# Performance work log

Hardware: AMD Instinct MI355X
Metric: run time of the kernel (lower is better)

Reference implementation:

```python
import jax, jax.numpy as jnp
import numpy as np

EPS = 0.1
MAX_ITER = 100
THRESH = 0.1


def setup_inputs() -> dict:
    key = jax.random.key(0)
    k1, k2, k3, k4 = jax.random.split(key, 4)
    N, P1, P2, D = 4, 1024, 1024, 16
    x = jax.random.normal(k1, (N, P1, D), dtype=jnp.float32)
    y = jax.random.normal(k2, (N, P2, D), dtype=jnp.float32)
    wx = jax.random.uniform(k3, (N, P1), dtype=jnp.float32)
    wy = jax.random.uniform(k4, (N, P2), dtype=jnp.float32)
    # normalize to probability weights (typical usage for empirical measures)
    wx = wx / jnp.sum(wx, axis=-1, keepdims=True)
    wy = wy / jnp.sum(wy, axis=-1, keepdims=True)
    return {"x": x, "y": y, "wx": wx, "wy": wy}


def _cost_matrix(x, y):
    # |x_i - y_j|^1 summed over feature dim -> [N, P1, P2]
    return jnp.sum(jnp.abs(x[:, :, None, :] - y[:, None, :, :]), axis=-1)


def reference(x, y, wx, wy):
    C = _cost_matrix(x, y)                     # [N, P1, P2]
    mu, nu = wx, wy                            # [N, P1], [N, P2]
    log_mu = jnp.log(mu + 1e-8)
    log_nu = jnp.log(nu + 1e-8)

    def M(u, v):
        # (-C_ij + u_i + v_j) / eps
        return (-C + u[:, :, None] + v[:, None, :]) / EPS

    def step(carry, _):
        u, v, done = carry
        u_new = EPS * (log_mu - jax.nn.logsumexp(M(u, v), axis=-1)) + u
        v_new = EPS * (log_nu - jax.nn.logsumexp(M(u_new, v), axis=-2)) + v
        err = jnp.mean(jnp.sum(jnp.abs(u_new - u), axis=-1))
        # emulate torch's early break: freeze u,v once converged
        u_out = jnp.where(done, u, u_new)
        v_out = jnp.where(done, v, v_new)
        done = done | (err < THRESH)
        return (u_out, v_out, done), None

    u0 = jnp.zeros_like(mu)
    v0 = jnp.zeros_like(nu)
    (u, v, _), _ = jax.lax.scan(step, (u0, v0, jnp.array(False)), None, length=MAX_ITER)

    pi = jnp.exp(M(u, v))                      # transport plan [N, P1, P2]
    cost = jnp.sum(pi * C, axis=(-2, -1))      # [N]  (reduction='none')
    return cost, pi, C
```

## Files before the change

kernel.cpp:

```cpp
#include <hip/hip_runtime.h>

static constexpr int   NB      = 4;
static constexpr int   PP      = 1024;
static constexpr int   DD      = 16;
static constexpr float EPSV    = 0.1f;
static constexpr float KE      = 14.42695041f;
static constexpr float KL      = 0.0693147181f;
static constexpr int   MAXIT   = 100;
static constexpr float THRESHV = 0.1f;

static constexpr int NBLK = 256;
static constexpr int NTHR = 512;
static constexpr unsigned DONEG = 1000000u;

static constexpr int    ERR_F_OFF     = 4352;
static constexpr size_t WS_ZERO_BYTES = 4352 * 4;
static constexpr size_t ERR_BYTES     = 512 * 4;

static constexpr int    VSNAP_OFF = 131072;
static constexpr int    CNT_F_OFF = 786432;
static constexpr size_t CNT_BYTES = (size_t)2 * MAXIT * 64;

__device__ __forceinline__ float fexp2(float v) { return __builtin_amdgcn_exp2f(v); }
__device__ __forceinline__ float flog2(float v) { return __builtin_amdgcn_logf(v); }

__device__ __forceinline__ float aload(const float* p) {
    return __hip_atomic_load(p, __ATOMIC_RELAXED, __HIP_MEMORY_SCOPE_AGENT);
}
__device__ __forceinline__ void astore(float* p, float v) {
    __hip_atomic_store(p, v, __ATOMIC_RELAXED, __HIP_MEMORY_SCOPE_AGENT);
}
__device__ __forceinline__ unsigned aloadu(const unsigned* p) {
    return __hip_atomic_load(p, __ATOMIC_RELAXED, __HIP_MEMORY_SCOPE_AGENT);
}
__device__ __forceinline__ void astoreu(unsigned* p, unsigned v) {
    __hip_atomic_store(p, v, __ATOMIC_RELAXED, __HIP_MEMORY_SCOPE_AGENT);
}
__device__ __forceinline__ float2 aload2(const float* p) {
    unsigned long long v = __hip_atomic_load((const unsigned long long*)p,
                                             __ATOMIC_RELAXED, __HIP_MEMORY_SCOPE_AGENT);
    union { unsigned long long u; float f[2]; } c; c.u = v;
    return make_float2(c.f[0], c.f[1]);
}
__device__ __forceinline__ void astore2(float* p, float a, float b) {
    union { unsigned long long u; float f[2]; } c; c.f[0] = a; c.f[1] = b;
    __hip_atomic_store((unsigned long long*)p, c.u,
                       __ATOMIC_RELAXED, __HIP_MEMORY_SCOPE_AGENT);
}
__device__ __forceinline__ void aadd(unsigned* p, unsigned v) {
    (void)__hip_atomic_fetch_add(p, v, __ATOMIC_RELAXED, __HIP_MEMORY_SCOPE_AGENT);
}

__device__ __forceinline__ void gbar_group(unsigned* ws32, int n, int g, unsigned gen) {
    __syncthreads();
    if (threadIdx.x < 64) {
        if (threadIdx.x == 0) astoreu(ws32 + (n * 64 + g) * 16, gen);
        const unsigned* sp = ws32 + (n * 64 + threadIdx.x) * 16;
        while (__ballot(aloadu(sp) >= gen) != ~0ull)
            __builtin_amdgcn_s_sleep(1);
    }
    __syncthreads();
}

__global__ __launch_bounds__(NTHR, 2)
void sinkhorn_kernel(const float* __restrict__ x, const float* __restrict__ y,
                     const float* __restrict__ wx, const float* __restrict__ wy,
                     float* __restrict__ out, float* __restrict__ ws)
{
    __shared__ float rt[16 * PP];
    __shared__ float sbuf[PP];
    __shared__ float cred[8];
    __shared__ int   Ts;
    __shared__ int   s_ex;
    __shared__ int   s_fired;

    unsigned* ws32  = (unsigned*)ws;
    unsigned* Tslot = ws32 + 4096;
    float*    ews   = ws + ERR_F_OFF;

    float* out_cost = out;
    float* out_pi   = out + NB;
    float* out_C    = out + NB + (size_t)NB * PP * PP;

    const int b   = blockIdx.x;
    const int n   = b >> 6;
    const int g   = b & 63;
    const int i0  = g * 16;
    const int w   = threadIdx.x >> 6;
    const int l   = threadIdx.x & 63;
    const int tid = threadIdx.x;

    float* sc = out_C + (size_t)n * PP * PP;
    unsigned* cnt = (unsigned*)(sc + CNT_F_OFF);

    if (tid == 0) { s_ex = 0; s_fired = 0; }

    float4 xr[2][4];
    #pragma unroll
    for (int rr = 0; rr < 2; ++rr) {
        const float4* xp = (const float4*)(x + ((size_t)n * PP + (i0 + 2 * w + rr)) * DD);
        #pragma unroll
        for (int q = 0; q < 4; ++q) xr[rr][q] = xp[q];
    }
    #pragma unroll 4
    for (int k = 0; k < 16; ++k) {
        int j = l + 64 * k;
        const float4* yp = (const float4*)(y + ((size_t)n * PP + j) * DD);
        float4 y0 = yp[0], y1 = yp[1], y2 = yp[2], y3 = yp[3];
        #pragma unroll
        for (int rr = 0; rr < 2; ++rr) {
            float c = fabsf(xr[rr][0].x - y0.x) + fabsf(xr[rr][0].y - y0.y)
                    + fabsf(xr[rr][0].z - y0.z) + fabsf(xr[rr][0].w - y0.w)
                    + fabsf(xr[rr][1].x - y1.x) + fabsf(xr[rr][1].y - y1.y)
                    + fabsf(xr[rr][1].z - y1.z) + fabsf(xr[rr][1].w - y1.w)
                    + fabsf(xr[rr][2].x - y2.x) + fabsf(xr[rr][2].y - y2.y)
                    + fabsf(xr[rr][2].z - y2.z) + fabsf(xr[rr][2].w - y2.w)
                    + fabsf(xr[rr][3].x - y3.x) + fabsf(xr[rr][3].y - y3.y)
                    + fabsf(xr[rr][3].z - y3.z) + fabsf(xr[rr][3].w - y3.w);
            rt[(2 * w + rr) * PP + j] = c;
        }
    }

    float4 yc[2][4];
    #pragma unroll
    for (int c = 0; c < 2; ++c) {
        const float4* yp = (const float4*)(y + ((size_t)n * PP + (i0 + 2 * w + c)) * DD);
        #pragma unroll
        for (int q = 0; q < 4; ++q) yc[c][q] = yp[q];
    }
    float2 c2[16];
    #pragma unroll 4
    for (int k = 0; k < 16; ++k) {
        const float4* xp = (const float4*)(x + ((size_t)n * PP + (l + 64 * k)) * DD);
        float4 x0 = xp[0], x1 = xp[1], x2 = xp[2], x3 = xp[3];
        float cc[2];
        #pragma unroll
        for (int c = 0; c < 2; ++c) {
            cc[c] = fabsf(x0.x - yc[c][0].x) + fabsf(x0.y - yc[c][0].y)
                  + fabsf(x0.z - yc[c][0].z) + fabsf(x0.w - yc[c][0].w)
                  + fabsf(x1.x - yc[c][1].x) + fabsf(x1.y - yc[c][1].y)
                  + fabsf(x1.z - yc[c][1].z) + fabsf(x1.w - yc[c][1].w)
                  + fabsf(x2.x - yc[c][2].x) + fabsf(x2.y - yc[c][2].y)
                  + fabsf(x2.z - yc[c][2].z) + fabsf(x2.w - yc[c][2].w)
                  + fabsf(x3.x - yc[c][3].x) + fabsf(x3.y - yc[c][3].y)
                  + fabsf(x3.z - yc[c][3].z) + fabsf(x3.w - yc[c][3].w);
        }
        c2[k] = make_float2(cc[0], cc[1]);
    }

    float lmu[2], lnu[2];
    #pragma unroll
    for (int rr = 0; rr < 2; ++rr) {
        lmu[rr] = __logf(wx[n * PP + i0 + 2 * w + rr] + 1e-8f);
        lnu[rr] = __logf(wy[n * PP + i0 + 2 * w + rr] + 1e-8f);
    }

    float uprev0 = 0.f, uprev1 = 0.f;

    #pragma unroll 1
    for (int t = 0; t < MAXIT; ++t) {
        if (t == 0) {
            sbuf[2 * tid] = 0.f; sbuf[2 * tid + 1] = 0.f;
        } else {
            if (tid == 0) {
                const unsigned* cp = cnt + (unsigned)(2 * (t - 1) + 1) * 16;
                unsigned cv;
                while (((cv = aloadu(cp)) & 0xFFFFu) != 64u)
                    __builtin_amdgcn_s_sleep(1);
                s_ex = (int)(cv >> 16);
            }
            __syncthreads();
            if (s_ex != 0) break;
            float2 vp = aload2(sc + VSNAP_OFF + (size_t)(t - 1) * PP + 2 * tid);
            sbuf[2 * tid] = vp.x; sbuf[2 * tid + 1] = vp.y;
        }
        __syncthreads();

        {
            float4 tt[2][4];
            float m0 = -3.4e38f, m1 = -3.4e38f;
            #pragma unroll
            for (int k = 0; k < 4; ++k) {
                int j = 256 * k + 4 * l;
                float4 v4 = *(const float4*)&sbuf[j];
                float4 ca = *(const float4*)&rt[(2 * w) * PP + j];
                float4 cb = *(const float4*)&rt[(2 * w + 1) * PP + j];
                tt[0][k] = make_float4(v4.x - ca.x, v4.y - ca.y, v4.z - ca.z, v4.w - ca.w);
                tt[1][k] = make_float4(v4.x - cb.x, v4.y - cb.y, v4.z - cb.z, v4.w - cb.w);
                m0 = fmaxf(m0, fmaxf(fmaxf(tt[0][k].x, tt[0][k].y), fmaxf(tt[0][k].z, tt[0][k].w)));
                m1 = fmaxf(m1, fmaxf(fmaxf(tt[1][k].x, tt[1][k].y), fmaxf(tt[1][k].z, tt[1][k].w)));
            }
            #pragma unroll
            for (int off = 32; off >= 1; off >>= 1) {
                m0 = fmaxf(m0, __shfl_xor(m0, off));
                m1 = fmaxf(m1, __shfl_xor(m1, off));
            }
            float s0 = 0.f, s1 = 0.f;
            #pragma unroll
            for (int k = 0; k < 4; ++k) {
                s0 += fexp2((tt[0][k].x - m0) * KE) + fexp2((tt[0][k].y - m0) * KE)
                    + fexp2((tt[0][k].z - m0) * KE) + fexp2((tt[0][k].w - m0) * KE);
                s1 += fexp2((tt[1][k].x - m1) * KE) + fexp2((tt[1][k].y - m1) * KE)
                    + fexp2((tt[1][k].z - m1) * KE) + fexp2((tt[1][k].w - m1) * KE);
            }
            #pragma unroll
            for (int off = 32; off >= 1; off >>= 1) {
                s0 += __shfl_xor(s0, off);
                s1 += __shfl_xor(s1, off);
            }
            float un0 = EPSV * lmu[0] - (m0 + KL * flog2(s0));
            float un1 = EPSV * lmu[1] - (m1 + KL * flog2(s1));
            if (l == 0) astore2(sc + (size_t)t * PP + i0 + 2 * w, un0, un1);
        }
        __syncthreads();
        if (tid == 0) {
            unsigned* cp = cnt + (unsigned)(2 * t) * 16;
            aadd(cp, 1u);
            while ((aloadu(cp) & 0xFFFFu) != 64u) __builtin_amdgcn_s_sleep(1);
        }
        __syncthreads();

        {
            float2 up = aload2(sc + (size_t)t * PP + 2 * tid);
            sbuf[2 * tid] = up.x; sbuf[2 * tid + 1] = up.y;
            float we = fabsf(up.x - uprev0) + fabsf(up.y - uprev1);
            uprev0 = up.x; uprev1 = up.y;
            #pragma unroll
            for (int off = 32; off >= 1; off >>= 1) we += __shfl_xor(we, off);
            if (l == 0) cred[w] = we;
        }
        __syncthreads();

        {
            float tt0[16], tt1[16], m0 = -3.4e38f, m1 = -3.4e38f;
            #pragma unroll
            for (int k = 0; k < 16; ++k) {
                float uu = sbuf[l + 64 * k];
                tt0[k] = uu - c2[k].x;
                tt1[k] = uu - c2[k].y;
                m0 = fmaxf(m0, tt0[k]);
                m1 = fmaxf(m1, tt1[k]);
            }
            #pragma unroll
            for (int off = 32; off >= 1; off >>= 1) {
                m0 = fmaxf(m0, __shfl_xor(m0, off));
                m1 = fmaxf(m1, __shfl_xor(m1, off));
            }
            float s0 = 0.f, s1 = 0.f;
            #pragma unroll
            for (int k = 0; k < 16; ++k) {
                s0 += fexp2((tt0[k] - m0) * KE);
                s1 += fexp2((tt1[k] - m1) * KE);
            }
            #pragma unroll
            for (int off = 32; off >= 1; off >>= 1) {
                s0 += __shfl_xor(s0, off);
                s1 += __shfl_xor(s1, off);
            }
            float vn0 = EPSV * lnu[0] - (m0 + KL * flog2(s0));
            float vn1 = EPSV * lnu[1] - (m1 + KL * flog2(s1));
            if (l == 0)
                astore2(sc + VSNAP_OFF + (size_t)t * PP + i0 + 2 * w, vn0, vn1);
        }
        if (g == 0 && tid == 0) {
            float es = cred[0] + cred[1] + cred[2] + cred[3]
                     + cred[4] + cred[5] + cred[6] + cred[7];
            astore(ews + n * 128 + t, es);
        }
        if (g == 0 && s_fired == 0 && tid < 64) {
            float esl = cred[0] + cred[1] + cred[2] + cred[3]
                      + cred[4] + cred[5] + cred[6] + cred[7];
            float s1f = 0.f, s2f = 0.f;
            #pragma unroll
            for (int q = 0; q < NB; ++q) {
                float e1 = aload(ews + q * 128 + tid);
                float e2 = aload(ews + q * 128 + 64 + tid);
                if (q == n) {
                    if (tid == t)      e1 = esl;
                    if (64 + tid == t) e2 = esl;
                }
                s1f += e1; s2f += e2;
            }
            unsigned long long bb = __ballot(s1f < THRESHV * (float)NB)
                                  | __ballot(s2f < THRESHV * (float)NB);
            if (tid == 0 && bb != 0ull) s_fired = 1;
        }

        __syncthreads();
        if (tid == 0) {
            unsigned addv = 1u + ((g == 0 && s_fired != 0) ? 65536u : 0u);
            aadd(cnt + (unsigned)(2 * t + 1) * 16, addv);
        }
    }

    if (g == 0 && tid == 0) astoreu(ws32 + (n * 64) * 16, DONEG);

    if (b == 0 && tid < 64) {
        for (;;) {
            bool ok = (tid >= 4) || (aloadu(ws32 + tid * 64 * 16) >= DONEG);
            if (__ballot(ok) == ~0ull) break;
            __builtin_amdgcn_s_sleep(2);
        }
        float s1f = aload(ews + 0 * 128 + tid) + aload(ews + 1 * 128 + tid)
                  + aload(ews + 2 * 128 + tid) + aload(ews + 3 * 128 + tid);
        float s2f = aload(ews + 0 * 128 + 64 + tid) + aload(ews + 1 * 128 + 64 + tid)
                  + aload(ews + 2 * 128 + 64 + tid) + aload(ews + 3 * 128 + 64 + tid);
        unsigned long long b1 = __ballot(s1f < THRESHV * (float)NB);
        unsigned long long b2 = __ballot(s2f < THRESHV * (float)NB);
        int T = b1 ? (__ffsll((long long)b1) - 1)
                   : (b2 ? 64 + (__ffsll((long long)b2) - 1) : MAXIT - 1);
        if (tid == 0) astoreu(Tslot, (unsigned)(T + 1));
    }
    if (tid == 0) {
        unsigned tv;
        while ((tv = aloadu(Tslot)) == 0u) __builtin_amdgcn_s_sleep(2);
        Ts = (int)tv - 1;
    }
    __syncthreads();
    const int T = Ts;

    float u_loc[2];
    {
        float2 up = aload2(sc + (size_t)T * PP + i0 + 2 * w);
        u_loc[0] = up.x; u_loc[1] = up.y;
        float2 vp = aload2(sc + VSNAP_OFF + (size_t)T * PP + 2 * tid);
        sbuf[2 * tid] = vp.x; sbuf[2 * tid + 1] = vp.y;
    }
    gbar_group(ws32, n, g, DONEG + 1u);

    float cacc = 0.f;
    #pragma unroll
    for (int rr = 0; rr < 2; ++rr) {
        int r = 2 * w + rr;
        int i = i0 + r;
        float un = u_loc[rr];
        #pragma unroll
        for (int k = 0; k < 4; ++k) {
            int j = 256 * k + 4 * l;
            float4 c4 = *(const float4*)&rt[r * PP + j];
            float4 v4 = *(const float4*)&sbuf[j];
            float4 p4;
            p4.x = fexp2((un + v4.x - c4.x) * KE);
            p4.y = fexp2((un + v4.y - c4.y) * KE);
            p4.z = fexp2((un + v4.z - c4.z) * KE);
            p4.w = fexp2((un + v4.w - c4.w) * KE);
            *(float4*)&out_pi[((size_t)n * PP + i) * PP + j] = p4;
            *(float4*)&out_C [((size_t)n * PP + i) * PP + j] = c4;
            cacc += p4.x * c4.x + p4.y * c4.y + p4.z * c4.z + p4.w * c4.w;
        }
    }
    #pragma unroll
    for (int off = 32; off >= 1; off >>= 1) cacc += __shfl_xor(cacc, off);
    if (l == 0) cred[w] = cacc;
    __syncthreads();
    if (tid == 0) {
        float s = 0.f;
        #pragma unroll
        for (int q = 0; q < 8; ++q) s += cred[q];
        atomicAdd(&out_cost[n], s);
    }
}

extern "C" void kernel_launch(void* const* d_in, const int* in_sizes, int n_in,
                              void* d_out, int out_size, void* d_ws, size_t ws_size,
                              hipStream_t stream) {
    const float* x  = (const float*)d_in[0];
    const float* y  = (const float*)d_in[1];
    const float* wx = (const float*)d_in[2];
    const float* wy = (const float*)d_in[3];
    float* out = (float*)d_out;
    float* ws  = (float*)d_ws;

    (void)hipMemsetAsync(d_ws, 0, WS_ZERO_BYTES, stream);
    (void)hipMemsetAsync((char*)d_ws + WS_ZERO_BYTES, 0x7f, ERR_BYTES, stream);
    (void)hipMemsetAsync(d_out, 0, NB * sizeof(float), stream);
    {
        size_t out_C_off = ((size_t)NB + (size_t)NB * PP * PP) * sizeof(float);
        size_t start = out_C_off + (size_t)CNT_F_OFF * sizeof(float);
        size_t span  = (size_t)(NB - 1) * PP * PP * sizeof(float) + CNT_BYTES;
        (void)hipMemsetAsync((char*)d_out + start, 0, span, stream);
    }

    hipLaunchKernelGGL(sinkhorn_kernel, dim3(NBLK), dim3(NTHR), 0, stream,
                       x, y, wx, wy, out, ws);
}
```

Before: 842.2 us.

## Replace counter barriers with NaN-sentinel dataflow sync and swizzled shared staging

Drops the per-iteration atomic counter barriers between the u and v half-steps. The snapshot buffers are now prefilled with 0xFF (NaN), and consumers poll until every value they need is non-NaN, so each block waits only on data arrival and not on a group-wide counter. Early exit now goes through a per-batch exit flag that blocks check with a one-iteration lag. Shared-memory staging of u and v uses XOR-swizzled indices to avoid bank conflicts. In exchange it adds a larger memset of the scratch area and spin polling on many addresses.

Result: slower. 998.0 us (+18.5%).

```diff
diff --git a/kernel.cpp b/kernel.cpp
--- a/kernel.cpp
+++ b/kernel.cpp
@@ -17,9 +17,8 @@
 static constexpr size_t WS_ZERO_BYTES = 4352 * 4;
 static constexpr size_t ERR_BYTES     = 512 * 4;
 
-static constexpr int    VSNAP_OFF = 131072;
-static constexpr int    CNT_F_OFF = 786432;
-static constexpr size_t CNT_BYTES = (size_t)2 * MAXIT * 64;
+static constexpr int SNAP_SHIFT = 12;
+static constexpr int VSNAP_OFF  = 131072;
 
 __device__ __forceinline__ float fexp2(float v) { return __builtin_amdgcn_exp2f(v); }
 __device__ __forceinline__ float flog2(float v) { return __builtin_amdgcn_logf(v); }
@@ -47,8 +46,40 @@
     __hip_atomic_store((unsigned long long*)p, c.u,
                        __ATOMIC_RELAXED, __HIP_MEMORY_SCOPE_AGENT);
 }
-__device__ __forceinline__ void aadd(unsigned* p, unsigned v) {
-    (void)__hip_atomic_fetch_add(p, v, __ATOMIC_RELAXED, __HIP_MEMORY_SCOPE_AGENT);
+
+
+__device__ __forceinline__ void stage_nan(const float* src, float* sbuf, int tid) {
+    if (tid < 64) {
+        const float* cp = src + tid * 16;
+        float2 d0, d1, d2, d3, d4, d5, d6, d7;
+        bool got = false;
+        for (;;) {
+            if (!got) {
+                float2 p7 = aload2(cp + 14);
+                if ((p7.x == p7.x) & (p7.y == p7.y)) {
+                    d0 = aload2(cp + 0);  d1 = aload2(cp + 2);
+                    d2 = aload2(cp + 4);  d3 = aload2(cp + 6);
+                    d4 = aload2(cp + 8);  d5 = aload2(cp + 10);
+                    d6 = aload2(cp + 12); d7 = p7;
+                    bool ok = (d0.x == d0.x) & (d0.y == d0.y)
+                            & (d1.x == d1.x) & (d1.y == d1.y)
+                            & (d2.x == d2.x) & (d2.y == d2.y)
+                            & (d3.x == d3.x) & (d3.y == d3.y)
+                            & (d4.x == d4.x) & (d4.y == d4.y)
+                            & (d5.x == d5.x) & (d5.y == d5.y)
+                            & (d6.x == d6.x) & (d6.y == d6.y);
+                    got = ok;
+                }
+            }
+            if (__ballot(got) == ~0ull) break;
+            __builtin_amdgcn_s_sleep(1);
+        }
+        const int base = 4 * tid, x7 = tid & 7;
+        *(float4*)&sbuf[4 * ((base + 0) ^ x7)] = make_float4(d0.x, d0.y, d1.x, d1.y);
+        *(float4*)&sbuf[4 * ((base + 1) ^ x7)] = make_float4(d2.x, d2.y, d3.x, d3.y);
+        *(float4*)&sbuf[4 * ((base + 2) ^ x7)] = make_float4(d4.x, d4.y, d5.x, d5.y);
+        *(float4*)&sbuf[4 * ((base + 3) ^ x7)] = make_float4(d6.x, d6.y, d7.x, d7.y);
+    }
 }
 
 __device__ __forceinline__ void gbar_group(unsigned* ws32, int n, int g, unsigned gen) {
@@ -69,13 +100,15 @@
 {
     __shared__ float rt[16 * PP];
     __shared__ float sbuf[PP];
+    __shared__ float g16[16];
     __shared__ float cred[8];
     __shared__ int   Ts;
-    __shared__ int   s_ex;
+    __shared__ int   s_ef;
     __shared__ int   s_fired;
 
     unsigned* ws32  = (unsigned*)ws;
     unsigned* Tslot = ws32 + 4096;
+    unsigned* exitf = ws32 + 4104;
     float*    ews   = ws + ERR_F_OFF;
 
     float* out_cost = out;
@@ -90,10 +123,26 @@
     const int l   = threadIdx.x & 63;
     const int tid = threadIdx.x;
 
-    float* sc = out_C + (size_t)n * PP * PP;
-    unsigned* cnt = (unsigned*)(sc + CNT_F_OFF);
-
-    if (tid == 0) { s_ex = 0; s_fired = 0; }
+    float* sc = out_C + (size_t)n * PP * PP + SNAP_SHIFT;
+
+    if (tid == 0) { s_ef = 0; s_fired = 0; }
+
+    int ru[4];
+    #pragma unroll
+    for (int k = 0; k < 4; ++k) ru[k] = 4 * (((64 * k) | l) ^ ((l >> 2) & 7));
+    int rv[16];
+    #pragma unroll
+    for (int k = 0; k < 16; ++k) {
+        int s = 16 * k + (l >> 2);
+        int p = s ^ ((4 * k + (l >> 4)) & 7);
+        rv[k] = 4 * p + (l & 3);
+    }
+    int ea;
+    {
+        int s = tid >> 1;
+        int p = s ^ ((tid >> 3) & 7);
+        ea = 4 * p + 2 * (tid & 1);
+    }
 
     float4 xr[2][4];
     #pragma unroll
@@ -159,20 +208,12 @@
 
     #pragma unroll 1
     for (int t = 0; t < MAXIT; ++t) {
+        if (t >= 2 && s_ef != 0 && t >= s_ef + 1) break;
+
         if (t == 0) {
-            sbuf[2 * tid] = 0.f; sbuf[2 * tid + 1] = 0.f;
+            sbuf[ea] = 0.f; sbuf[ea + 1] = 0.f;
         } else {
-            if (tid == 0) {
-                const unsigned* cp = cnt + (unsigned)(2 * (t - 1) + 1) * 16;
-                unsigned cv;
-                while (((cv = aloadu(cp)) & 0xFFFFu) != 64u)
-                    __builtin_amdgcn_s_sleep(1);
-                s_ex = (int)(cv >> 16);
-            }
-            __syncthreads();
-            if (s_ex != 0) break;
-            float2 vp = aload2(sc + VSNAP_OFF + (size_t)(t - 1) * PP + 2 * tid);
-            sbuf[2 * tid] = vp.x; sbuf[2 * tid + 1] = vp.y;
+            stage_nan(sc + VSNAP_OFF + (size_t)(t - 1) * PP, sbuf, tid);
         }
         __syncthreads();
 
@@ -182,7 +223,7 @@
             #pragma unroll
             for (int k = 0; k < 4; ++k) {
                 int j = 256 * k + 4 * l;
-                float4 v4 = *(const float4*)&sbuf[j];
+                float4 v4 = *(const float4*)&sbuf[ru[k]];
                 float4 ca = *(const float4*)&rt[(2 * w) * PP + j];
                 float4 cb = *(const float4*)&rt[(2 * w + 1) * PP + j];
                 tt[0][k] = make_float4(v4.x - ca.x, v4.y - ca.y, v4.z - ca.z, v4.w - ca.w);
@@ -210,21 +251,23 @@
             }
             float un0 = EPSV * lmu[0] - (m0 + KL * flog2(s0));
             float un1 = EPSV * lmu[1] - (m1 + KL * flog2(s1));
-            if (l == 0) astore2(sc + (size_t)t * PP + i0 + 2 * w, un0, un1);
+            if (l == 0) { g16[2 * w] = un0; g16[2 * w + 1] = un1; }
         }
         __syncthreads();
         if (tid == 0) {
-            unsigned* cp = cnt + (unsigned)(2 * t) * 16;
-            aadd(cp, 1u);
-            while ((aloadu(cp) & 0xFFFFu) != 64u) __builtin_amdgcn_s_sleep(1);
-        }
+            float* up = sc + (size_t)t * PP + i0;
+            #pragma unroll
+            for (int q = 0; q < 8; ++q)
+                astore2(up + 2 * q, g16[2 * q], g16[2 * q + 1]);
+        }
+
+        stage_nan(sc + (size_t)t * PP, sbuf, tid);
         __syncthreads();
 
         {
-            float2 up = aload2(sc + (size_t)t * PP + 2 * tid);
-            sbuf[2 * tid] = up.x; sbuf[2 * tid + 1] = up.y;
-            float we = fabsf(up.x - uprev0) + fabsf(up.y - uprev1);
-            uprev0 = up.x; uprev1 = up.y;
+            float up0 = sbuf[ea], up1 = sbuf[ea + 1];
+            float we = fabsf(up0 - uprev0) + fabsf(up1 - uprev1);
+            uprev0 = up0; uprev1 = up1;
             #pragma unroll
             for (int off = 32; off >= 1; off >>= 1) we += __shfl_xor(we, off);
             if (l == 0) cred[w] = we;
@@ -235,7 +278,7 @@
             float tt0[16], tt1[16], m0 = -3.4e38f, m1 = -3.4e38f;
             #pragma unroll
             for (int k = 0; k < 16; ++k) {
-                float uu = sbuf[l + 64 * k];
+                float uu = sbuf[rv[k]];
                 tt0[k] = uu - c2[k].x;
                 tt1[k] = uu - c2[k].y;
                 m0 = fmaxf(m0, tt0[k]);
@@ -259,13 +302,19 @@
             }
             float vn0 = EPSV * lnu[0] - (m0 + KL * flog2(s0));
             float vn1 = EPSV * lnu[1] - (m1 + KL * flog2(s1));
-            if (l == 0)
-                astore2(sc + VSNAP_OFF + (size_t)t * PP + i0 + 2 * w, vn0, vn1);
-        }
-        if (g == 0 && tid == 0) {
-            float es = cred[0] + cred[1] + cred[2] + cred[3]
-                     + cred[4] + cred[5] + cred[6] + cred[7];
-            astore(ews + n * 128 + t, es);
+            if (l == 0) { g16[2 * w] = vn0; g16[2 * w + 1] = vn1; }
+        }
+        __syncthreads();
+        if (tid == 0) {
+            if (g == 0) {
+                float es = cred[0] + cred[1] + cred[2] + cred[3]
+                         + cred[4] + cred[5] + cred[6] + cred[7];
+                astore(ews + n * 128 + t, es);
+            }
+            float* vp = sc + VSNAP_OFF + (size_t)t * PP + i0;
+            #pragma unroll
+            for (int q = 0; q < 8; ++q)
+                astore2(vp + 2 * q, g16[2 * q], g16[2 * q + 1]);
         }
         if (g == 0 && s_fired == 0 && tid < 64) {
             float esl = cred[0] + cred[1] + cred[2] + cred[3]
@@ -283,14 +332,13 @@
             }
             unsigned long long bb = __ballot(s1f < THRESHV * (float)NB)
                                   | __ballot(s2f < THRESHV * (float)NB);
-            if (tid == 0 && bb != 0ull) s_fired = 1;
-        }
-
-        __syncthreads();
-        if (tid == 0) {
-            unsigned addv = 1u + ((g == 0 && s_fired != 0) ? 65536u : 0u);
-            aadd(cnt + (unsigned)(2 * t + 1) * 16, addv);
-        }
+            if (tid == 0 && bb != 0ull) {
+                astoreu(exitf + n, (unsigned)(t + 1));
+                s_fired = 1;
+            }
+        }
+        if (tid == 0) s_ef = (int)aloadu(exitf + n);
+        __syncthreads();
     }
 
     if (g == 0 && tid == 0) astoreu(ws32 + (n * 64) * 16, DONEG);
@@ -321,10 +369,14 @@
 
     float u_loc[2];
     {
-        float2 up = aload2(sc + (size_t)T * PP + i0 + 2 * w);
+        const float* upp = sc + (size_t)T * PP + i0 + 2 * w;
+        float2 up;
+        do { up = aload2(upp); } while ((up.x != up.x) | (up.y != up.y));
         u_loc[0] = up.x; u_loc[1] = up.y;
-        float2 vp = aload2(sc + VSNAP_OFF + (size_t)T * PP + 2 * tid);
-        sbuf[2 * tid] = vp.x; sbuf[2 * tid + 1] = vp.y;
+        const float* vpp = sc + VSNAP_OFF + (size_t)T * PP + 2 * tid;
+        float2 vp;
+        do { vp = aload2(vpp); } while ((vp.x != vp.x) | (vp.y != vp.y));
+        sbuf[ea] = vp.x; sbuf[ea + 1] = vp.y;
     }
     gbar_group(ws32, n, g, DONEG + 1u);
 
@@ -338,7 +390,7 @@
         for (int k = 0; k < 4; ++k) {
             int j = 256 * k + 4 * l;
             float4 c4 = *(const float4*)&rt[r * PP + j];
-            float4 v4 = *(const float4*)&sbuf[j];
+            float4 v4 = *(const float4*)&sbuf[ru[k]];
             float4 p4;
             p4.x = fexp2((un + v4.x - c4.x) * KE);
             p4.y = fexp2((un + v4.y - c4.y) * KE);
@@ -376,9 +428,9 @@
     (void)hipMemsetAsync(d_out, 0, NB * sizeof(float), stream);
     {
         size_t out_C_off = ((size_t)NB + (size_t)NB * PP * PP) * sizeof(float);
-        size_t start = out_C_off + (size_t)CNT_F_OFF * sizeof(float);
-        size_t span  = (size_t)(NB - 1) * PP * PP * sizeof(float) + CNT_BYTES;
-        (void)hipMemsetAsync((char*)d_out + start, 0, span, stream);
+        size_t span = (size_t)(NB - 1) * PP * PP * sizeof(float)
+                    + ((size_t)SNAP_SHIFT + VSNAP_OFF + (size_t)MAXIT * PP) * sizeof(float);
+        (void)hipMemsetAsync((char*)d_out + out_C_off, 0xFF, span, stream);
     }
 
     hipLaunchKernelGGL(sinkhorn_kernel, dim3(NBLK), dim3(NTHR), 0, stream,
```
